# Optimization experiments

Hardware: AMD Instinct MI355X
Metric: run time of the kernel (lower is better)

The kernel has to match this reference:

```python
import jax, jax.numpy as jnp
import numpy as np

NE, NR = 100000, 50
E, H, M = 512, 8, 8
HD = E // H
B = 65536


def setup_inputs() -> dict:
    key = jax.random.key(0)
    ks = jax.random.split(key, 24)
    xav = lambda k, shp: jax.random.normal(k, shp, jnp.float32) * (2.0 / (shp[0] + shp[-1])) ** 0.5
    return {
        'entity_emb': xav(ks[0], (NE, E)),
        'relation_emb': xav(ks[1], (NR, E)),
        'dens_ent_emb': jax.random.normal(ks[2], (NE, E), jnp.float32) * 0.02,
        'dens_ent_w': xav(ks[3], (E, 1)), 'dens_ent_b': jnp.zeros((1,), jnp.float32),
        'dens_rel_emb': jax.random.normal(ks[4], (NR, E), jnp.float32) * 0.02,
        'dens_rel_w': xav(ks[5], (E, 1)), 'dens_rel_b': jnp.zeros((1,), jnp.float32),
        'local_motifs': xav(ks[6], (M, HD)),
        'global_motifs': xav(ks[7], (M, HD)),
        'Wq': xav(ks[8], (E, E)), 'bq': jnp.zeros((E,), jnp.float32),
        'Wkl': xav(ks[9], (HD, HD)), 'bkl': jnp.zeros((HD,), jnp.float32),
        'Wkg': xav(ks[10], (HD, HD)), 'bkg': jnp.zeros((HD,), jnp.float32),
        'Wout': xav(ks[11], (2 * E, E)), 'bout': jnp.zeros((E,), jnp.float32),
        'adv_w': jnp.float32(1.0), 'adv_b': jnp.float32(0.0),
        'h_idx': jax.random.randint(ks[12], (B,), 0, NE),
        'r_idx': jax.random.randint(ks[13], (B,), 0, NR),
        't_idx': jax.random.randint(ks[14], (B,), 0, NE),
    }


def reference(entity_emb, relation_emb, dens_ent_emb, dens_ent_w, dens_ent_b,
              dens_rel_emb, dens_rel_w, dens_rel_b, local_motifs, global_motifs,
              Wq, bq, Wkl, bkl, Wkg, bkg, Wout, bout, adv_w, adv_b,
              h_idx, r_idx, t_idx):
    h = entity_emb[h_idx]           # [B, E]
    r = relation_emb[r_idx]
    t = entity_emb[t_idx]
    # density gating: sigmoid(Linear(Embedding(idx))) per head/tail/relation, averaged
    h_d = jax.nn.sigmoid(dens_ent_emb[h_idx] @ dens_ent_w + dens_ent_b)   # [B,1]
    t_d = jax.nn.sigmoid(dens_ent_emb[t_idx] @ dens_ent_w + dens_ent_b)
    r_d = jax.nn.sigmoid(dens_rel_emb[r_idx] @ dens_rel_w + dens_rel_b)
    density = (h_d + t_d + r_d) / 3.0                                     # [B,1]
    diff = h + r - t
    # hierarchical soft attention over local/global motif codebooks
    ctx = h + r + t
    q = (ctx @ Wq + bq).reshape(-1, H, HD)                                # [B,H,HD]
    lk = local_motifs @ Wkl + bkl                                         # [M,HD]
    gk = global_motifs @ Wkg + bkg
    scale = 1.0 / jnp.sqrt(jnp.asarray(HD, q.dtype))
    dens = density[:, :, None]                                            # [B,1,1]
    l_w = jax.nn.softmax(jnp.einsum('bhd,md->bhm', q, lk) * scale + dens, axis=-1)
    g_w = jax.nn.softmax(jnp.einsum('bhd,md->bhm', q, gk) * scale + dens, axis=-1)
    attn = (l_w + g_w) / 2.0                                              # [B,H,M]
    motifs = local_motifs + global_motifs                                 # [M,HD]
    motif_repr = jnp.einsum('bhm,md->bhd', attn, motifs).reshape(-1, E)   # [B,E]
    motif_loss = jnp.sum((diff - motif_repr) ** 2, axis=-1)               # ||.||^2
    combined = jnp.concatenate([diff, motif_repr], axis=-1)               # [B,2E]
    transformed = jnp.tanh(combined @ Wout + bout)
    score = adv_w * jnp.linalg.norm(transformed, axis=-1) + adv_b
    return score, motif_loss
```

## Files before the change

kernel.cpp:

```cpp
#include <hip/hip_runtime.h>
#include <math.h>

#define B_TOT 65536

typedef __attribute__((ext_vector_type(4))) float f32x4;
typedef __attribute__((ext_vector_type(4))) unsigned int u32x4;
typedef __attribute__((ext_vector_type(8))) __bf16 bf16x8;

#define OFF_WLOGT 0u
#define OFF_CBIAS 131072u
#define OFF_BCAT  131584u
#define OFF_MOTIF 721408u
#define OFF_LK    723456u
#define OFF_GK    725504u
#define OFF_DIFF  1048576u
#define OFF_ATTN  68157440u
#define OFF_SSQ   76546048u

__device__ __forceinline__ unsigned short f2bf(float x) {
  union { float f; unsigned int u; } v; v.f = x;
  return (unsigned short)((v.u + 0x7FFFu + ((v.u >> 16) & 1u)) >> 16);
}

__device__ __forceinline__ float bf2f(unsigned short u) {
  union { unsigned int i; float f; } v; v.i = ((unsigned int)u) << 16; return v.f;
}

__device__ __forceinline__ float fast_tanh(float x) {
  float cx = fminf(fmaxf(x, -15.f), 15.f);
  float e = __expf(2.f * cx);
  return 1.f - 2.f * __builtin_amdgcn_rcpf(e + 1.f);
}

__global__ __launch_bounds__(256) void k0a(
    const float* __restrict__ lm, const float* __restrict__ gm,
    const float* __restrict__ Wkl, const float* __restrict__ bkl,
    const float* __restrict__ Wkg, const float* __restrict__ bkg,
    const float* __restrict__ bq,
    float* __restrict__ lk, float* __restrict__ gk,
    float* __restrict__ motifs, float* __restrict__ cb) {
  int tid = threadIdx.x;
  for (int o = tid; o < 512; o += 256) {
    int m = o >> 6, d = o & 63;
    float s1 = bkl[d], s2 = bkg[d];
    for (int k = 0; k < 64; ++k) {
      s1 += lm[m*64+k] * Wkl[k*64+d];
      s2 += gm[m*64+k] * Wkg[k*64+d];
    }
    lk[o] = s1; gk[o] = s2;
    motifs[o] = lm[o] + gm[o];
  }
  __syncthreads();
  if (tid < 128) {
    int s_ = tid >> 6, h = (tid >> 3) & 7, m = tid & 7;
    const float* K = s_ ? gk : lk;
    float s = 0.f;
    for (int d = 0; d < 64; ++d) s += bq[h*64+d] * K[m*64+d];
    cb[tid] = 0.125f * s;
  }
}

__global__ __launch_bounds__(256) void k0b(
    const float* __restrict__ Wq, const float* __restrict__ Wout,
    const float* __restrict__ lk, const float* __restrict__ gk,
    const float* __restrict__ motifs,
    unsigned short* __restrict__ wlogT, unsigned short* __restrict__ bcatT) {
  int idx = blockIdx.x * 256 + threadIdx.x;
  if (idx >= 65536 + 512*576) return;
  if (idx < 65536) {
    int c = idx >> 9, k = idx & 511;
    int s_ = c >> 6, h = (c >> 3) & 7, m = c & 7;
    const float* K = (s_ ? gk : lk) + m*64;
    const float* wq = Wq + (size_t)k*512 + h*64;
    float s = 0.f;
    for (int d = 0; d < 64; ++d) s += wq[d] * K[d];
    wlogT[(size_t)c*512 + k] = f2bf(0.125f * s);
  } else {
    int i2 = idx - 65536;
    int n = i2 / 576, k = i2 - n*576;
    float v;
    if (k < 512) {
      v = Wout[(size_t)k*512 + n];
    } else {
      int hm = k - 512, h = hm >> 3, m = hm & 7;
      const float* mo = motifs + m*64;
      const float* wo = Wout + (size_t)(512 + h*64)*512 + n;
      v = 0.f;
      for (int d = 0; d < 64; ++d) v += mo[d] * wo[(size_t)d*512];
    }
    bcatT[(size_t)n*576 + k] = f2bf(v);
  }
}

__global__ __launch_bounds__(256, 6) void kA(
    const float* __restrict__ ent, const float* __restrict__ rel,
    const int* __restrict__ hI, const int* __restrict__ rI, const int* __restrict__ tI,
    const unsigned short* __restrict__ wlogT, const float* __restrict__ cb,
    unsigned short* __restrict__ diffB, unsigned short* __restrict__ attnB) {
  __shared__ __align__(16) unsigned char smem[23040];
  unsigned short* As = (unsigned short*)smem;
  unsigned short* Bs = (unsigned short*)(smem + 4608);
  float* lg  = (float*)smem;

  int tid = threadIdx.x;
  int l = tid & 63, wc = tid >> 6;
  int rowBase = blockIdx.x * 32;
  int r_loc = tid >> 3, p = tid & 7;
  int b = rowBase + r_loc;

  int hi = hI[b], ri = rI[b], ti = tI[b];
  const float* hp = ent + (size_t)hi * 512;
  const float* tp = ent + (size_t)ti * 512;
  const float* rp = rel + (size_t)ri * 512;
  int bn = tid >> 1, half = tid & 1;
  const unsigned short* wsrc = wlogT + (size_t)bn * 512 + half * 32;

  f32x4 acc[2][2] = {};

  float4 gh[2], gt[2], gr[2];
  u32x4 wb[4];

  {
    int q0 = p*8;
    gh[0] = *(const float4*)(hp + q0); gh[1] = *(const float4*)(hp + q0 + 4);
    gt[0] = *(const float4*)(tp + q0); gt[1] = *(const float4*)(tp + q0 + 4);
    gr[0] = *(const float4*)(rp + q0); gr[1] = *(const float4*)(rp + q0 + 4);
    #pragma unroll
    for (int o = 0; o < 4; ++o) wb[o] = *(const u32x4*)(wsrc + o*8);
  }

  #pragma unroll
  for (int c = 0; c < 8; ++c) {
    int k0 = c * 64;
    union { u32x4 v; unsigned short s[8]; } pd, pc;
    #pragma unroll
    for (int g = 0; g < 2; ++g) {
      #pragma unroll
      for (int j = 0; j < 4; ++j) {
        float hv = ((const float*)&gh[g])[j];
        float tv = ((const float*)&gt[g])[j];
        float rv = ((const float*)&gr[g])[j];
        pd.s[g*4+j] = f2bf(hv + rv - tv);
        pc.s[g*4+j] = f2bf(hv + rv + tv);
      }
    }

    __syncthreads();
    *(u32x4*)(As + r_loc*72 + p*8) = pc.v;
    {
      unsigned short* bp = Bs + bn*72 + half*32;
      *(u32x4*)(bp)      = wb[0];
      *(u32x4*)(bp + 8)  = wb[1];
      *(u32x4*)(bp + 16) = wb[2];
      *(u32x4*)(bp + 24) = wb[3];
    }
    *(u32x4*)(diffB + (size_t)b*512 + k0 + p*8) = pd.v;
    __syncthreads();
    if (c < 7) {
      int q0 = k0 + 64 + p*8;
      gh[0] = *(const float4*)(hp + q0); gh[1] = *(const float4*)(hp + q0 + 4);
      gt[0] = *(const float4*)(tp + q0); gt[1] = *(const float4*)(tp + q0 + 4);
      gr[0] = *(const float4*)(rp + q0); gr[1] = *(const float4*)(rp + q0 + 4);
      #pragma unroll
      for (int o = 0; o < 4; ++o) wb[o] = *(const u32x4*)(wsrc + (c+1)*64 + o*8);
    }
    #pragma unroll
    for (int kf = 0; kf < 2; ++kf) {
      bf16x8 af0 = *(const bf16x8*)(As + (     (l & 15))*72 + kf*32 + 8*(l >> 4));
      bf16x8 af1 = *(const bf16x8*)(As + (16 + (l & 15))*72 + kf*32 + 8*(l >> 4));
      #pragma unroll
      for (int n = 0; n < 2; ++n) {
        int col = wc*32 + n*16 + (l & 15);
        bf16x8 bfr = *(const bf16x8*)(Bs + col*72 + kf*32 + 8*(l >> 4));
        acc[0][n] = __builtin_amdgcn_mfma_f32_16x16x32_bf16(af0, bfr, acc[0][n], 0, 0, 0);
        acc[1][n] = __builtin_amdgcn_mfma_f32_16x16x32_bf16(af1, bfr, acc[1][n], 0, 0, 0);
      }
    }
  }

  __syncthreads();
  #pragma unroll
  for (int m = 0; m < 2; ++m)
    #pragma unroll
    for (int n = 0; n < 2; ++n)
      #pragma unroll
      for (int j = 0; j < 4; ++j) {
        int rr = m*16 + 4*(l >> 4) + j;
        int cc = wc*32 + n*16 + (l & 15);
        lg[rr*128 + ((cc + rr) & 127)] = acc[m][n][j];
      }
  __syncthreads();

  {
    float a8[8];
    #pragma unroll
    for (int m = 0; m < 8; ++m) a8[m] = 0.f;
    #pragma unroll
    for (int s = 0; s < 2; ++s) {
      float v[8], mx = -1e30f;
      #pragma unroll
      for (int m = 0; m < 8; ++m) {
        int cc = s*64 + p*8 + m;
        v[m] = lg[r_loc*128 + ((cc + r_loc) & 127)] + cb[cc];
        mx = fmaxf(mx, v[m]);
      }
      float sum = 0.f;
      #pragma unroll
      for (int m = 0; m < 8; ++m) { v[m] = __expf(v[m] - mx); sum += v[m]; }
      float inv = 0.5f / sum;
      #pragma unroll
      for (int m = 0; m < 8; ++m) a8[m] += v[m] * inv;
    }
    union { u32x4 v; unsigned short s[8]; } pk;
    #pragma unroll
    for (int m = 0; m < 8; ++m) pk.s[m] = f2bf(a8[m]);
    *(u32x4*)(attnB + (size_t)b*64 + p*8) = pk.v;
  }
}

__global__ __launch_bounds__(512, 4) void kB(
    const unsigned short* __restrict__ diffB, const unsigned short* __restrict__ attnB,
    const unsigned short* __restrict__ bcatT, const float* __restrict__ bout,
    float* __restrict__ ssqPart) {
  __shared__ __align__(16) unsigned short As[128*72];
  __shared__ __align__(16) unsigned short Bs[256*72];
  __shared__ float part[128*4];
  int tid = threadIdx.x;
  int l = tid & 63, wid = tid >> 6;
  int wr = wid >> 2, wc = wid & 3;
  int mblk = blockIdx.x >> 1, nblk = blockIdx.x & 1;
  int rowBase = mblk * 128;
  int colBase = nblk * 256;
  f32x4 acc[4][4] = {};
  int ar = tid >> 2, aq = tid & 3;
  int bn2 = tid >> 1, half = tid & 1;

  u32x4 na0, na1, nb0, nb1, nb2, nb3;
  {
    const unsigned short* ap = diffB + (size_t)(rowBase + ar)*512 + aq*16;
    na0 = *(const u32x4*)ap; na1 = *(const u32x4*)(ap + 8);
    const u32x4* src = (const u32x4*)(bcatT + (size_t)(colBase + bn2)*576 + half*32);
    nb0 = src[0]; nb1 = src[1]; nb2 = src[2]; nb3 = src[3];
  }
  for (int ks = 0; ks < 9; ++ks) {
    __syncthreads();
    *(u32x4*)(&As[ar*72 + aq*16])     = na0;
    *(u32x4*)(&As[ar*72 + aq*16 + 8]) = na1;
    {
      unsigned short* bp = &Bs[bn2*72 + half*32];
      *(u32x4*)(bp)      = nb0;
      *(u32x4*)(bp + 8)  = nb1;
      *(u32x4*)(bp + 16) = nb2;
      *(u32x4*)(bp + 24) = nb3;
    }
    __syncthreads();
    if (ks < 8) {
      int k0 = (ks + 1) * 64;
      const unsigned short* ap = (k0 < 512)
        ? diffB + (size_t)(rowBase + ar)*512 + k0 + aq*16
        : attnB + (size_t)(rowBase + ar)*64 + aq*16;
      na0 = *(const u32x4*)ap; na1 = *(const u32x4*)(ap + 8);
      const u32x4* src = (const u32x4*)(bcatT + (size_t)(colBase + bn2)*576 + k0 + half*32);
      nb0 = src[0]; nb1 = src[1]; nb2 = src[2]; nb3 = src[3];
    }
    #pragma unroll
    for (int kf = 0; kf < 2; ++kf) {
      bf16x8 af[4];
      #pragma unroll
      for (int m = 0; m < 4; ++m)
        af[m] = *(const bf16x8*)(&As[(wr*64 + m*16 + (l & 15))*72 + kf*32 + 8*(l >> 4)]);
      #pragma unroll
      for (int n = 0; n < 4; ++n) {
        bf16x8 bfr = *(const bf16x8*)(&Bs[(wc*64 + n*16 + (l & 15))*72 + kf*32 + 8*(l >> 4)]);
        #pragma unroll
        for (int m = 0; m < 4; ++m)
          acc[m][n] = __builtin_amdgcn_mfma_f32_16x16x32_bf16(af[m], bfr, acc[m][n], 0, 0, 0);
      }
    }
  }
  __syncthreads();
  float bo[4];
  #pragma unroll
  for (int n = 0; n < 4; ++n) bo[n] = bout[colBase + wc*64 + n*16 + (l & 15)];
  #pragma unroll
  for (int m = 0; m < 4; ++m) {
    float ss0 = 0.f, ss1 = 0.f, ss2 = 0.f, ss3 = 0.f;
    #pragma unroll
    for (int n = 0; n < 4; ++n) {
      float t0 = fast_tanh(acc[m][n][0] + bo[n]); ss0 += t0*t0;
      float t1 = fast_tanh(acc[m][n][1] + bo[n]); ss1 += t1*t1;
      float t2 = fast_tanh(acc[m][n][2] + bo[n]); ss2 += t2*t2;
      float t3 = fast_tanh(acc[m][n][3] + bo[n]); ss3 += t3*t3;
    }
    #pragma unroll
    for (int mask = 1; mask < 16; mask <<= 1) {
      ss0 += __shfl_xor(ss0, mask, 64);
      ss1 += __shfl_xor(ss1, mask, 64);
      ss2 += __shfl_xor(ss2, mask, 64);
      ss3 += __shfl_xor(ss3, mask, 64);
    }
    if ((l & 15) == 0) {
      int rbase = wr*64 + m*16 + (l >> 4)*4;
      part[(rbase+0)*4 + wc] = ss0;
      part[(rbase+1)*4 + wc] = ss1;
      part[(rbase+2)*4 + wc] = ss2;
      part[(rbase+3)*4 + wc] = ss3;
    }
  }
  __syncthreads();
  if (tid < 128) {
    float s = part[tid*4] + part[tid*4+1] + part[tid*4+2] + part[tid*4+3];
    ssqPart[(size_t)nblk*B_TOT + rowBase + tid] = s;
  }
}

__global__ __launch_bounds__(256) void kCD(
    const unsigned short* __restrict__ diffB, const unsigned short* __restrict__ attnB,
    const float* __restrict__ motifs, const float* __restrict__ ssqPart,
    const float* __restrict__ advw, const float* __restrict__ advb,
    float* __restrict__ lossOut, float* __restrict__ scoreOut) {
  __shared__ float mo[512];
  int tid = threadIdx.x;
  mo[tid] = motifs[tid];
  mo[tid + 256] = motifs[tid + 256];
  __syncthreads();
  int l = tid & 63;
  int b = blockIdx.x * 4 + (tid >> 6);
  union { u32x4 v; unsigned short s[8]; } dv, av;
  dv.v = *(const u32x4*)(diffB + (size_t)b*512 + l*8);
  int h = l >> 3;
  av.v = *(const u32x4*)(attnB + (size_t)b*64 + h*8);
  float at[8], df[8];
  #pragma unroll
  for (int j = 0; j < 8; ++j) { df[j] = bf2f(dv.s[j]); at[j] = bf2f(av.s[j]); }
  int dbase = (l & 7) * 8;
  float part = 0.f;
  #pragma unroll
  for (int j = 0; j < 8; ++j) {
    float repr = 0.f;
    #pragma unroll
    for (int m = 0; m < 8; ++m) repr += at[m] * mo[m*64 + dbase + j];
    float e = df[j] - repr;
    part += e * e;
  }
  #pragma unroll
  for (int off = 1; off < 64; off <<= 1) part += __shfl_xor(part, off, 64);
  if (l == 0) lossOut[b] = part;
  if (tid < 4) {
    int rb = blockIdx.x * 4 + tid;
    float s = ssqPart[rb] + ssqPart[B_TOT + rb];
    scoreOut[rb] = advw[0] * sqrtf(s) + advb[0];
  }
}

extern "C" void kernel_launch(void* const* d_in, const int* in_sizes, int n_in,
                              void* d_out, int out_size, void* d_ws, size_t ws_size,
                              hipStream_t stream) {
  const float* ent  = (const float*)d_in[0];
  const float* rel  = (const float*)d_in[1];
  const float* lm   = (const float*)d_in[8];
  const float* gm   = (const float*)d_in[9];
  const float* Wq   = (const float*)d_in[10];
  const float* bq   = (const float*)d_in[11];
  const float* Wkl  = (const float*)d_in[12];
  const float* bkl  = (const float*)d_in[13];
  const float* Wkg  = (const float*)d_in[14];
  const float* bkg  = (const float*)d_in[15];
  const float* Wout = (const float*)d_in[16];
  const float* bout = (const float*)d_in[17];
  const float* advw = (const float*)d_in[18];
  const float* advb = (const float*)d_in[19];
  const int* hI = (const int*)d_in[20];
  const int* rI = (const int*)d_in[21];
  const int* tI = (const int*)d_in[22];
  char* ws = (char*)d_ws;
  unsigned short* wlogT = (unsigned short*)(ws + OFF_WLOGT);
  float* cb     = (float*)(ws + OFF_CBIAS);
  unsigned short* bcatT = (unsigned short*)(ws + OFF_BCAT);
  float* motifs = (float*)(ws + OFF_MOTIF);
  float* lk     = (float*)(ws + OFF_LK);
  float* gk     = (float*)(ws + OFF_GK);
  unsigned short* diffB = (unsigned short*)(ws + OFF_DIFF);
  unsigned short* attnB = (unsigned short*)(ws + OFF_ATTN);
  float* ssqPart = (float*)(ws + OFF_SSQ);
  float* scoreOut = (float*)d_out;
  float* lossOut  = (float*)d_out + B_TOT;

  hipLaunchKernelGGL(k0a, dim3(1), dim3(256), 0, stream,
                     lm, gm, Wkl, bkl, Wkg, bkg, bq, lk, gk, motifs, cb);
  hipLaunchKernelGGL(k0b, dim3(1408), dim3(256), 0, stream,
                     Wq, Wout, lk, gk, motifs, wlogT, bcatT);
  hipLaunchKernelGGL(kA, dim3(B_TOT/32), dim3(256), 0, stream,
                     ent, rel, hI, rI, tI, wlogT, cb, diffB, attnB);
  hipLaunchKernelGGL(kB, dim3(B_TOT/128 * 2), dim3(512), 0, stream,
                     diffB, attnB, bcatT, bout, ssqPart);
  hipLaunchKernelGGL(kCD, dim3(B_TOT/4), dim3(256), 0, stream,
                     diffB, attnB, motifs, ssqPart, advw, advb, lossOut, scoreOut);
}
```

Before: 151.1 us.

## Restructure kA so each wave owns 16 rows and loads MFMA fragments directly

New measurement: 202.0 us. +33.7%, slower.

```diff
diff --git a/kernel.cpp b/kernel.cpp
--- a/kernel.cpp
+++ b/kernel.cpp
@@ -92,129 +92,91 @@
   }
 }
 
-__global__ __launch_bounds__(256, 6) void kA(
+__global__ __launch_bounds__(256, 4) void kA(
     const float* __restrict__ ent, const float* __restrict__ rel,
     const int* __restrict__ hI, const int* __restrict__ rI, const int* __restrict__ tI,
     const unsigned short* __restrict__ wlogT, const float* __restrict__ cb,
     unsigned short* __restrict__ diffB, unsigned short* __restrict__ attnB) {
-  __shared__ __align__(16) unsigned char smem[23040];
-  unsigned short* As = (unsigned short*)smem;
-  unsigned short* Bs = (unsigned short*)(smem + 4608);
-  float* lg  = (float*)smem;
+  __shared__ unsigned short attnStage[4][16*64];
 
   int tid = threadIdx.x;
-  int l = tid & 63, wc = tid >> 6;
-  int rowBase = blockIdx.x * 32;
-  int r_loc = tid >> 3, p = tid & 7;
-  int b = rowBase + r_loc;
+  int l = tid & 63, wid = tid >> 6;
+  int rowBase = (blockIdx.x * 4 + wid) * 16;
+  int r16 = l & 15;
+  int kg = l >> 4;
+  int b = rowBase + r16;
 
   int hi = hI[b], ri = rI[b], ti = tI[b];
   const float* hp = ent + (size_t)hi * 512;
   const float* tp = ent + (size_t)ti * 512;
   const float* rp = rel + (size_t)ri * 512;
-  int bn = tid >> 1, half = tid & 1;
-  const unsigned short* wsrc = wlogT + (size_t)bn * 512 + half * 32;
-
-  f32x4 acc[2][2] = {};
-
-  float4 gh[2], gt[2], gr[2];
-  u32x4 wb[4];
-
-  {
-    int q0 = p*8;
-    gh[0] = *(const float4*)(hp + q0); gh[1] = *(const float4*)(hp + q0 + 4);
-    gt[0] = *(const float4*)(tp + q0); gt[1] = *(const float4*)(tp + q0 + 4);
-    gr[0] = *(const float4*)(rp + q0); gr[1] = *(const float4*)(rp + q0 + 4);
-    #pragma unroll
-    for (int o = 0; o < 4; ++o) wb[o] = *(const u32x4*)(wsrc + o*8);
-  }
-
-  #pragma unroll
+  const unsigned short* wbase = wlogT + (size_t)r16 * 512 + kg * 8;
+
+  f32x4 acc[8] = {};
+
   for (int c = 0; c < 8; ++c) {
     int k0 = c * 64;
-    union { u32x4 v; unsigned short s[8]; } pd, pc;
-    #pragma unroll
-    for (int g = 0; g < 2; ++g) {
+    int q0 = k0 + kg*8, q1 = k0 + 32 + kg*8;
+    float hv[16], tv[16], rv[16];
+    *(float4*)&hv[0]  = *(const float4*)(hp + q0); *(float4*)&hv[4]  = *(const float4*)(hp + q0 + 4);
+    *(float4*)&hv[8]  = *(const float4*)(hp + q1); *(float4*)&hv[12] = *(const float4*)(hp + q1 + 4);
+    *(float4*)&tv[0]  = *(const float4*)(tp + q0); *(float4*)&tv[4]  = *(const float4*)(tp + q0 + 4);
+    *(float4*)&tv[8]  = *(const float4*)(tp + q1); *(float4*)&tv[12] = *(const float4*)(tp + q1 + 4);
+    *(float4*)&rv[0]  = *(const float4*)(rp + q0); *(float4*)&rv[4]  = *(const float4*)(rp + q0 + 4);
+    *(float4*)&rv[8]  = *(const float4*)(rp + q1); *(float4*)&rv[12] = *(const float4*)(rp + q1 + 4);
+
+    union { bf16x8 v; unsigned short s[8]; } a0, a1;
+    union { u32x4 v; unsigned short s[8]; } d0, d1;
+    #pragma unroll
+    for (int j = 0; j < 8; ++j) {
+      float hr0 = hv[j]   + rv[j],   hr1 = hv[8+j] + rv[8+j];
+      a0.s[j] = f2bf(hr0 + tv[j]);   d0.s[j] = f2bf(hr0 - tv[j]);
+      a1.s[j] = f2bf(hr1 + tv[8+j]); d1.s[j] = f2bf(hr1 - tv[8+j]);
+    }
+    *(u32x4*)(diffB + (size_t)b*512 + q0) = d0.v;
+    *(u32x4*)(diffB + (size_t)b*512 + q1) = d1.v;
+
+    #pragma unroll
+    for (int n = 0; n < 8; ++n) {
+      const unsigned short* wp = wbase + (size_t)n*16*512 + k0;
+      bf16x8 b0 = *(const bf16x8*)(wp);
+      bf16x8 b1 = *(const bf16x8*)(wp + 32);
+      acc[n] = __builtin_amdgcn_mfma_f32_16x16x32_bf16(a0.v, b0, acc[n], 0, 0, 0);
+      acc[n] = __builtin_amdgcn_mfma_f32_16x16x32_bf16(a1.v, b1, acc[n], 0, 0, 0);
+    }
+  }
+
+  float cbv[8];
+  #pragma unroll
+  for (int n = 0; n < 8; ++n) cbv[n] = cb[n*16 + r16];
+
+  #pragma unroll
+  for (int j = 0; j < 4; ++j) {
+    int rloc = kg*4 + j;
+    float w[8];
+    #pragma unroll
+    for (int n = 0; n < 8; ++n) {
+      float v = acc[n][j] + cbv[n];
+      float mx = v;
       #pragma unroll
-      for (int j = 0; j < 4; ++j) {
-        float hv = ((const float*)&gh[g])[j];
-        float tv = ((const float*)&gt[g])[j];
-        float rv = ((const float*)&gr[g])[j];
-        pd.s[g*4+j] = f2bf(hv + rv - tv);
-        pc.s[g*4+j] = f2bf(hv + rv + tv);
-      }
-    }
-
-    __syncthreads();
-    *(u32x4*)(As + r_loc*72 + p*8) = pc.v;
-    {
-      unsigned short* bp = Bs + bn*72 + half*32;
-      *(u32x4*)(bp)      = wb[0];
-      *(u32x4*)(bp + 8)  = wb[1];
-      *(u32x4*)(bp + 16) = wb[2];
-      *(u32x4*)(bp + 24) = wb[3];
-    }
-    *(u32x4*)(diffB + (size_t)b*512 + k0 + p*8) = pd.v;
-    __syncthreads();
-    if (c < 7) {
-      int q0 = k0 + 64 + p*8;
-      gh[0] = *(const float4*)(hp + q0); gh[1] = *(const float4*)(hp + q0 + 4);
-      gt[0] = *(const float4*)(tp + q0); gt[1] = *(const float4*)(tp + q0 + 4);
-      gr[0] = *(const float4*)(rp + q0); gr[1] = *(const float4*)(rp + q0 + 4);
+      for (int mk = 1; mk < 8; mk <<= 1) mx = fmaxf(mx, __shfl_xor(mx, mk, 64));
+      float e = __expf(v - mx);
+      float s = e;
       #pragma unroll
-      for (int o = 0; o < 4; ++o) wb[o] = *(const u32x4*)(wsrc + (c+1)*64 + o*8);
-    }
-    #pragma unroll
-    for (int kf = 0; kf < 2; ++kf) {
-      bf16x8 af0 = *(const bf16x8*)(As + (     (l & 15))*72 + kf*32 + 8*(l >> 4));
-      bf16x8 af1 = *(const bf16x8*)(As + (16 + (l & 15))*72 + kf*32 + 8*(l >> 4));
-      #pragma unroll
-      for (int n = 0; n < 2; ++n) {
-        int col = wc*32 + n*16 + (l & 15);
-        bf16x8 bfr = *(const bf16x8*)(Bs + col*72 + kf*32 + 8*(l >> 4));
-        acc[0][n] = __builtin_amdgcn_mfma_f32_16x16x32_bf16(af0, bfr, acc[0][n], 0, 0, 0);
-        acc[1][n] = __builtin_amdgcn_mfma_f32_16x16x32_bf16(af1, bfr, acc[1][n], 0, 0, 0);
-      }
-    }
-  }
-
-  __syncthreads();
-  #pragma unroll
-  for (int m = 0; m < 2; ++m)
-    #pragma unroll
-    for (int n = 0; n < 2; ++n)
-      #pragma unroll
-      for (int j = 0; j < 4; ++j) {
-        int rr = m*16 + 4*(l >> 4) + j;
-        int cc = wc*32 + n*16 + (l & 15);
-        lg[rr*128 + ((cc + rr) & 127)] = acc[m][n][j];
-      }
-  __syncthreads();
+      for (int mk = 1; mk < 8; mk <<= 1) s += __shfl_xor(s, mk, 64);
+      w[n] = e / s;
+    }
+    #pragma unroll
+    for (int n = 0; n < 4; ++n)
+      attnStage[wid][rloc*64 + n*16 + r16] = f2bf(0.5f * (w[n] + w[n+4]));
+  }
 
   {
-    float a8[8];
-    #pragma unroll
-    for (int m = 0; m < 8; ++m) a8[m] = 0.f;
-    #pragma unroll
-    for (int s = 0; s < 2; ++s) {
-      float v[8], mx = -1e30f;
-      #pragma unroll
-      for (int m = 0; m < 8; ++m) {
-        int cc = s*64 + p*8 + m;
-        v[m] = lg[r_loc*128 + ((cc + r_loc) & 127)] + cb[cc];
-        mx = fmaxf(mx, v[m]);
-      }
-      float sum = 0.f;
-      #pragma unroll
-      for (int m = 0; m < 8; ++m) { v[m] = __expf(v[m] - mx); sum += v[m]; }
-      float inv = 0.5f / sum;
-      #pragma unroll
-      for (int m = 0; m < 8; ++m) a8[m] += v[m] * inv;
-    }
-    union { u32x4 v; unsigned short s[8]; } pk;
-    #pragma unroll
-    for (int m = 0; m < 8; ++m) pk.s[m] = f2bf(a8[m]);
-    *(u32x4*)(attnB + (size_t)b*64 + p*8) = pk.v;
+    int rr = l >> 2, off = (l & 3) * 16;
+    const u32x4* src = (const u32x4*)(&attnStage[wid][rr*64 + off]);
+    u32x4 w0 = src[0], w1 = src[1];
+    u32x4* dst = (u32x4*)(attnB + (size_t)(rowBase + rr)*64 + off);
+    dst[0] = w0; dst[1] = w1;
   }
 }
 
@@ -390,7 +352,7 @@
                      lm, gm, Wkl, bkl, Wkg, bkg, bq, lk, gk, motifs, cb);
   hipLaunchKernelGGL(k0b, dim3(1408), dim3(256), 0, stream,
                      Wq, Wout, lk, gk, motifs, wlogT, bcatT);
-  hipLaunchKernelGGL(kA, dim3(B_TOT/32), dim3(256), 0, stream,
+  hipLaunchKernelGGL(kA, dim3(B_TOT/64), dim3(256), 0, stream,
                      ent, rel, hI, rI, tI, wlogT, cb, diffB, attnB);
   hipLaunchKernelGGL(kB, dim3(B_TOT/128 * 2), dim3(512), 0, stream,
                      diffB, attnB, bcatT, bout, ssqPart);
```
